# Optimization experiments

Measured on AMD Instinct MI355X. Metric: run time of the kernel, lower is better.

The kernel has to match this reference:

```python
import jax, jax.numpy as jnp
import numpy as np

ALPHA = 0.2  # leaky relu slope

def setup_inputs() -> dict:
    key = jax.random.key(0)
    k1, k2, k3, k4 = jax.random.split(key, 4)
    b, n, din, dout = 8, 2048, 256, 128
    x = jax.random.normal(k1, (b, n, din), dtype=jnp.float32)
    adj = jax.random.randint(k2, (b, n, n), 0, 2, dtype=jnp.int32)
    # xavier-ish scaling for params
    W = jax.random.normal(k3, (dout, din), dtype=jnp.float32) * (1.414 * (2.0 / (din + dout)) ** 0.5)
    a = jax.random.normal(k4, (2 * dout,), dtype=jnp.float32) * (1.414 * (2.0 / (2 * dout + 1)) ** 0.5)
    return {"x": x, "adj": adj, "W": W, "a": a}

def reference(x, adj, W, a):
    # x: [b, n, din]; W: [dout, din]; a: [2*dout]
    wh = jnp.einsum('bnd,od->bno', x, W)           # [b, n, dout]
    dout = W.shape[0]
    a_src, a_dst = a[:dout], a[dout:]
    # e_ij = leaky_relu(a_src . wh_i + a_dst . wh_j)  (decomposed, avoids O(n^2 * 2d) concat)
    e = (wh @ a_src)[:, :, None] + (wh @ a_dst)[:, None, :]  # [b, n, n]
    e = jnp.where(e >= 0, e, ALPHA * e)
    e = jnp.where(adj != 0, e, -jnp.inf)
    attention = jax.nn.softmax(e, axis=2)          # [b, n, n]
    out = jnp.einsum('bij,bjo->bio', attention, wh)  # [b, n, dout]
    return jax.nn.relu(out)
```

## Files before the change

kernel.cpp:

```cpp
#include <hip/hip_runtime.h>
#include <hip/hip_bf16.h>
#include <stdint.h>

#define GAT_ALPHA 0.2f
#define LOG2E 1.4426950408889634f

typedef __attribute__((ext_vector_type(8))) __bf16 bf16x8;
typedef __attribute__((ext_vector_type(4))) float f32x4;

union B8 {
  bf16x8 b;
  unsigned short u[8];
  unsigned int w[4];
  int4 i4;
};

__device__ __forceinline__ unsigned int pk2bf(float lo, float hi) {
  union { __hip_bfloat162 h; unsigned int u; } cv;
  cv.h = __float22bfloat162_rn(make_float2(lo, hi));
  return cv.u;
}

__global__ __launch_bounds__(256) void gat_pack(
    const int* __restrict__ adj, unsigned long long* __restrict__ mask) {
  const int tid = threadIdx.x;
  const int lane = tid & 63;
  const int wgl = (blockIdx.x * 256 + tid) >> 6;
  for (int it = wgl; it < 131072; it += 4096) {
    const size_t base = (size_t)it << 8;
    const int* p = adj + base + lane;
    int a0 = p[0], a1 = p[64], a2 = p[128], a3 = p[192];
    unsigned long long m0 = __ballot(a0 != 0);
    unsigned long long m1 = __ballot(a1 != 0);
    unsigned long long m2 = __ballot(a2 != 0);
    unsigned long long m3 = __ballot(a3 != 0);
    if (lane == 0) {
      unsigned long long* mp = mask + (base >> 6);
      mp[0] = m0; mp[1] = m1; mp[2] = m2; mp[3] = m3;
    }
  }
}

__global__ __launch_bounds__(256, 2) void gat_wh(
    const float* __restrict__ x, const float* __restrict__ W,
    const float* __restrict__ a, unsigned short* __restrict__ whTf,
    float* __restrict__ s_out, float* __restrict__ d_out) {
  __shared__ unsigned short WF[8][4][512];
  const int tid = threadIdx.x;
  const int wave = tid >> 6, lane = tid & 63;
  const int il = lane & 15, quad = lane >> 4;
  const int row0 = blockIdx.x * 64;
  const int i = row0 + wave * 16 + il;
  B8 av[8];
  {
    const float* xp = x + (size_t)i * 256 + quad * 8;
#pragma unroll
    for (int kc = 0; kc < 8; ++kc) {
      float4 lo = *(const float4*)(xp + kc * 32);
      float4 hi = *(const float4*)(xp + kc * 32 + 4);
      av[kc].w[0] = pk2bf(lo.x, lo.y);
      av[kc].w[1] = pk2bf(lo.z, lo.w);
      av[kc].w[2] = pk2bf(hi.x, hi.y);
      av[kc].w[3] = pk2bf(hi.z, hi.w);
    }
  }
  f32x4 acc[8];
#pragma unroll
  for (int nt = 0; nt < 8; ++nt) acc[nt] = (f32x4){0.f, 0.f, 0.f, 0.f};
#pragma unroll
  for (int h = 0; h < 2; ++h) {
    if (h) __syncthreads();
#pragma unroll
    for (int p = 0; p < 16; ++p) {
      const int f = p * 1024 + tid * 4;
      const int o = f >> 7, kk = f & 127;
      float4 v = *(const float4*)(W + o * 256 + h * 128 + kk);
      uint2 pk;
      pk.x = pk2bf(v.x, v.y);
      pk.y = pk2bf(v.z, v.w);
      *(uint2*)(&WF[o >> 4][kk >> 5][((o & 15) + (((kk & 31) >> 3) << 4)) * 8 + (kk & 7)]) = pk;
    }
    __syncthreads();
#pragma unroll
    for (int kl = 0; kl < 4; ++kl) {
      const int kc = h * 4 + kl;
#pragma unroll
      for (int nt = 0; nt < 8; ++nt) {
        B8 bv;
        bv.i4 = *(const int4*)(&WF[nt][kl][lane * 8]);
        acc[nt] = __builtin_amdgcn_mfma_f32_16x16x32_bf16(av[kc].b, bv.b, acc[nt], 0, 0, 0);
      }
    }
  }
  float asrc[8], adst[8];
#pragma unroll
  for (int nt = 0; nt < 8; ++nt) {
    asrc[nt] = a[nt * 16 + il];
    adst[nt] = a[128 + nt * 16 + il];
  }
  float sp[4], dp[4];
#pragma unroll
  for (int r = 0; r < 4; ++r) {
    float sv = 0.f, dv = 0.f;
#pragma unroll
    for (int nt = 0; nt < 8; ++nt) {
      sv += acc[nt][r] * asrc[nt];
      dv += acc[nt][r] * adst[nt];
    }
    sp[r] = sv; dp[r] = dv;
  }
#pragma unroll
  for (int off = 1; off <= 8; off <<= 1) {
#pragma unroll
    for (int r = 0; r < 4; ++r) {
      sp[r] += __shfl_xor(sp[r], off, 64);
      dp[r] += __shfl_xor(dp[r], off, 64);
    }
  }
  if (il == 0) {
#pragma unroll
    for (int r = 0; r < 4; ++r) {
      s_out[row0 + wave * 16 + quad * 4 + r] = sp[r];
      d_out[row0 + wave * 16 + quad * 4 + r] = dp[r];
    }
  }
  const int b = row0 >> 11;
  const int jc = ((row0 & 2047) >> 5) + (wave >> 1);
  const int kin = ((wave & 1) << 4) + (quad << 2);
  const int kq = kin >> 3, u0 = kin & 7;
#pragma unroll
  for (int nt = 0; nt < 8; ++nt) {
    uint2 pk;
    pk.x = pk2bf(acc[nt][0], acc[nt][1]);
    pk.y = pk2bf(acc[nt][2], acc[nt][3]);
    *(uint2*)(whTf + ((((size_t)(b * 64 + jc)) * 8 + nt) << 9) + ((il + (kq << 4)) << 3) + u0) = pk;
  }
}

__device__ __forceinline__ void dma16(const void* g, void* l) {
  __builtin_amdgcn_global_load_lds(
      (const __attribute__((address_space(1))) unsigned int*)g,
      (__attribute__((address_space(3))) unsigned int*)l, 16, 0, 0);
}

__global__ __launch_bounds__(256) void gat_attn(
    const unsigned int* __restrict__ mask32, const unsigned short* __restrict__ whTf,
    const float* __restrict__ s, const float* __restrict__ dvec,
    float* __restrict__ out) {
  __shared__ unsigned short vbuf[2][2][8][512];
  __shared__ unsigned int maskl[64][68];
  __shared__ float dl[2048];
  const int tid = threadIdx.x;
  const int wave = tid >> 6;
  const int lane = tid & 63;
  const int il = lane & 15;
  const int quad = lane >> 4;
  const int qo = quad << 3;
  const int b = blockIdx.x & 7;
  const int tile = blockIdx.x >> 3;
  const int rbase = tile * 64;
  {
    const float* dsrc = dvec + ((size_t)b << 11);
#pragma unroll
    for (int it = 0; it < 2; ++it) {
      const int idx = it * 1024 + tid * 4;
      float4 v = *(const float4*)(dsrc + idx);
      v.x *= LOG2E; v.y *= LOG2E; v.z *= LOG2E; v.w *= LOG2E;
      *(float4*)(&dl[idx]) = v;
    }
  }
  {
    const unsigned int* msrc = mask32 + (((size_t)b << 11) + rbase) * 64;
    const int c4 = (tid & 15) << 2;
#pragma unroll
    for (int kk = 0; kk < 4; ++kk) {
      const int r = (tid >> 4) + kk * 16;
      *(int4*)(&maskl[r][c4]) = *(const int4*)(msrc + r * 64 + c4);
    }
  }
  const unsigned short* whTb = whTf + (((size_t)b * 64) << 12);
  {
#pragma unroll
    for (int h = 0; h < 2; ++h) {
      const int nt = wave * 2 + h;
      dma16(whTb + ((size_t)(0 * 8 + nt) << 9) + (lane << 3), &vbuf[0][0][nt][0]);
      dma16(whTb + ((size_t)(1 * 8 + nt) << 9) + (lane << 3), &vbuf[0][1][nt][0]);
    }
  }
  const int i = rbase + wave * 16 + il;
  const size_t browi = ((size_t)b << 11) + i;
  const float svL = s[browi] * LOG2E;
  const int mrow = wave * 16 + il;

  f32x4 acc[8];
#pragma unroll
  for (int nt = 0; nt < 8; ++nt) acc[nt] = (f32x4){0.f, 0.f, 0.f, 0.f};
  float den = 0.f;
  __syncthreads();

#pragma unroll 2
  for (int T = 0; T < 32; ++T) {
    const int cur = T & 1, nxt = cur ^ 1;
    if (T < 31) {
#pragma unroll
      for (int h = 0; h < 2; ++h) {
        const int nt = wave * 2 + h;
        dma16(whTb + (((size_t)(2 * T + 2) * 8 + nt) << 9) + (lane << 3), &vbuf[nxt][0][nt][0]);
        dma16(whTb + (((size_t)(2 * T + 3) * 8 + nt) << 9) + (lane << 3), &vbuf[nxt][1][nt][0]);
      }
    }
#pragma unroll
    for (int c = 0; c < 2; ++c) {
      const int tt = 2 * T + c;
      const int j0 = tt * 32;
      const unsigned int mword = maskl[mrow][tt];
      const float4 d0 = *(const float4*)(&dl[j0 + qo]);
      const float4 d1 = *(const float4*)(&dl[j0 + qo + 4]);
      const float dd[8] = {d0.x, d0.y, d0.z, d0.w, d1.x, d1.y, d1.z, d1.w};
      B8 af[8];
#pragma unroll
      for (int nt = 0; nt < 8; ++nt)
        af[nt].i4 = *(const int4*)((const char*)&vbuf[cur][c][nt][0] + lane * 16);
      float pv[8];
#pragma unroll
      for (int u = 0; u < 8; ++u) {
        float t0 = svL + dd[u];
        float e2 = fmaxf(t0, GAT_ALPHA * t0);
        float p = __builtin_amdgcn_exp2f(e2);
        p = ((mword >> (qo + u)) & 1u) ? p : 0.f;
        den += p;
        pv[u] = p;
      }
      B8 pf;
      pf.w[0] = pk2bf(pv[0], pv[1]);
      pf.w[1] = pk2bf(pv[2], pv[3]);
      pf.w[2] = pk2bf(pv[4], pv[5]);
      pf.w[3] = pk2bf(pv[6], pv[7]);
#pragma unroll
      for (int nt = 0; nt < 8; ++nt)
        acc[nt] = __builtin_amdgcn_mfma_f32_16x16x32_bf16(af[nt].b, pf.b, acc[nt], 0, 0, 0);
    }
    __syncthreads();
  }
  den += __shfl_xor(den, 16, 64);
  den += __shfl_xor(den, 32, 64);
  const float inv = 1.0f / den;
  float* op = out + browi * 128;
#pragma unroll
  for (int nt = 0; nt < 8; ++nt) {
    float4 v;
    v.x = fmaxf(acc[nt][0] * inv, 0.f);
    v.y = fmaxf(acc[nt][1] * inv, 0.f);
    v.z = fmaxf(acc[nt][2] * inv, 0.f);
    v.w = fmaxf(acc[nt][3] * inv, 0.f);
    *(float4*)(op + nt * 16 + quad * 4) = v;
  }
}

extern "C" void kernel_launch(void* const* d_in, const int* in_sizes, int n_in,
                              void* d_out, int out_size, void* d_ws, size_t ws_size,
                              hipStream_t stream) {
  const float* x = (const float*)d_in[0];
  const int* adj = (const int*)d_in[1];
  const float* W = (const float*)d_in[2];
  const float* a = (const float*)d_in[3];
  float* out = (float*)d_out;
  unsigned short* whTf = (unsigned short*)d_ws;
  unsigned long long* mask = (unsigned long long*)((char*)d_ws + (size_t)4 * 1024 * 1024);
  float* s = (float*)((char*)d_ws + (size_t)8 * 1024 * 1024);
  float* dv = s + 16384;
  gat_pack<<<1024, 256, 0, stream>>>(adj, mask);
  gat_wh<<<256, 256, 0, stream>>>(x, W, a, whTf, s, dv);
  gat_attn<<<256, 256, 0, stream>>>((const unsigned int*)mask, whTf, s, dv, out);
}
```

Measured before the change: 255.5 us.

## Fuse adjacency bitmask packing into attention kernel, reading adj directly

Removes the separate gat_pack kernel and its mask buffer. The attention kernel now loads the int32 adjacency rows itself, one 64-column chunk per iteration, prefetching the next chunk into registers, and builds per-row bitmasks with wave ballots. This saves a kernel launch and the write and read of the packed mask. In exchange, the 128 MB adjacency read now sits inside the attention loop and adds 16 ballots per iteration, and the previous unroll-2 pragma is dropped.

```diff
diff --git a/kernel.cpp b/kernel.cpp
--- a/kernel.cpp
+++ b/kernel.cpp
@@ -21,24 +21,10 @@
   return cv.u;
 }
 
-__global__ __launch_bounds__(256) void gat_pack(
-    const int* __restrict__ adj, unsigned long long* __restrict__ mask) {
-  const int tid = threadIdx.x;
-  const int lane = tid & 63;
-  const int wgl = (blockIdx.x * 256 + tid) >> 6;
-  for (int it = wgl; it < 131072; it += 4096) {
-    const size_t base = (size_t)it << 8;
-    const int* p = adj + base + lane;
-    int a0 = p[0], a1 = p[64], a2 = p[128], a3 = p[192];
-    unsigned long long m0 = __ballot(a0 != 0);
-    unsigned long long m1 = __ballot(a1 != 0);
-    unsigned long long m2 = __ballot(a2 != 0);
-    unsigned long long m3 = __ballot(a3 != 0);
-    if (lane == 0) {
-      unsigned long long* mp = mask + (base >> 6);
-      mp[0] = m0; mp[1] = m1; mp[2] = m2; mp[3] = m3;
-    }
-  }
+__device__ __forceinline__ void dma16(const void* g, void* l) {
+  __builtin_amdgcn_global_load_lds(
+      (const __attribute__((address_space(1))) unsigned int*)g,
+      (__attribute__((address_space(3))) unsigned int*)l, 16, 0, 0);
 }
 
 __global__ __launch_bounds__(256, 2) void gat_wh(
@@ -137,18 +123,11 @@
   }
 }
 
-__device__ __forceinline__ void dma16(const void* g, void* l) {
-  __builtin_amdgcn_global_load_lds(
-      (const __attribute__((address_space(1))) unsigned int*)g,
-      (__attribute__((address_space(3))) unsigned int*)l, 16, 0, 0);
-}
-
 __global__ __launch_bounds__(256) void gat_attn(
-    const unsigned int* __restrict__ mask32, const unsigned short* __restrict__ whTf,
+    const int* __restrict__ adj, const unsigned short* __restrict__ whTf,
     const float* __restrict__ s, const float* __restrict__ dvec,
     float* __restrict__ out) {
   __shared__ unsigned short vbuf[2][2][8][512];
-  __shared__ unsigned int maskl[64][68];
   __shared__ float dl[2048];
   const int tid = threadIdx.x;
   const int wave = tid >> 6;
@@ -169,15 +148,10 @@
       *(float4*)(&dl[idx]) = v;
     }
   }
-  {
-    const unsigned int* msrc = mask32 + (((size_t)b << 11) + rbase) * 64;
-    const int c4 = (tid & 15) << 2;
-#pragma unroll
-    for (int kk = 0; kk < 4; ++kk) {
-      const int r = (tid >> 4) + kk * 16;
-      *(int4*)(&maskl[r][c4]) = *(const int4*)(msrc + r * 64 + c4);
-    }
-  }
+  const int* aro = adj + ((((size_t)b << 11) + rbase + wave * 16) << 11);
+  int lv[16];
+#pragma unroll
+  for (int r = 0; r < 16; ++r) lv[r] = aro[(r << 11) + lane];
   const unsigned short* whTb = whTf + (((size_t)b * 64) << 12);
   {
 #pragma unroll
@@ -190,18 +164,27 @@
   const int i = rbase + wave * 16 + il;
   const size_t browi = ((size_t)b << 11) + i;
   const float svL = s[browi] * LOG2E;
-  const int mrow = wave * 16 + il;
-
+  unsigned long long mcur;
+  {
+    unsigned long long sel = __ballot(lv[0] != 0);
+#pragma unroll
+    for (int r = 1; r < 16; ++r) {
+      const unsigned long long mm = __ballot(lv[r] != 0);
+      sel = (il == r) ? mm : sel;
+    }
+    mcur = sel;
+  }
   f32x4 acc[8];
 #pragma unroll
   for (int nt = 0; nt < 8; ++nt) acc[nt] = (f32x4){0.f, 0.f, 0.f, 0.f};
   float den = 0.f;
   __syncthreads();
 
-#pragma unroll 2
   for (int T = 0; T < 32; ++T) {
     const int cur = T & 1, nxt = cur ^ 1;
     if (T < 31) {
+#pragma unroll
+      for (int r = 0; r < 16; ++r) lv[r] = aro[(r << 11) + (T + 1) * 64 + lane];
 #pragma unroll
       for (int h = 0; h < 2; ++h) {
         const int nt = wave * 2 + h;
@@ -211,9 +194,8 @@
     }
 #pragma unroll
     for (int c = 0; c < 2; ++c) {
-      const int tt = 2 * T + c;
-      const int j0 = tt * 32;
-      const unsigned int mword = maskl[mrow][tt];
+      const int j0 = (2 * T + c) * 32;
+      const unsigned int mq = (unsigned int)(mcur >> (32 * c + qo));
       const float4 d0 = *(const float4*)(&dl[j0 + qo]);
       const float4 d1 = *(const float4*)(&dl[j0 + qo + 4]);
       const float dd[8] = {d0.x, d0.y, d0.z, d0.w, d1.x, d1.y, d1.z, d1.w};
@@ -227,7 +209,7 @@
         float t0 = svL + dd[u];
         float e2 = fmaxf(t0, GAT_ALPHA * t0);
         float p = __builtin_amdgcn_exp2f(e2);
-        p = ((mword >> (qo + u)) & 1u) ? p : 0.f;
+        p = ((mq >> u) & 1u) ? p : 0.f;
         den += p;
         pv[u] = p;
       }
@@ -239,6 +221,15 @@
 #pragma unroll
       for (int nt = 0; nt < 8; ++nt)
         acc[nt] = __builtin_amdgcn_mfma_f32_16x16x32_bf16(af[nt].b, pf.b, acc[nt], 0, 0, 0);
+    }
+    if (T < 31) {
+      unsigned long long sel = __ballot(lv[0] != 0);
+#pragma unroll
+      for (int r = 1; r < 16; ++r) {
+        const unsigned long long mm = __ballot(lv[r] != 0);
+        sel = (il == r) ? mm : sel;
+      }
+      mcur = sel;
     }
     __syncthreads();
   }
@@ -266,10 +257,8 @@
   const float* a = (const float*)d_in[3];
   float* out = (float*)d_out;
   unsigned short* whTf = (unsigned short*)d_ws;
-  unsigned long long* mask = (unsigned long long*)((char*)d_ws + (size_t)4 * 1024 * 1024);
-  float* s = (float*)((char*)d_ws + (size_t)8 * 1024 * 1024);
+  float* s = (float*)((char*)d_ws + (size_t)4 * 1024 * 1024);
   float* dv = s + 16384;
-  gat_pack<<<1024, 256, 0, stream>>>(adj, mask);
   gat_wh<<<256, 256, 0, stream>>>(x, W, a, whTf, s, dv);
-  gat_attn<<<256, 256, 0, stream>>>((const unsigned int*)mask, whTf, s, dv, out);
-}
+  gat_attn<<<256, 256, 0, stream>>>(adj, whTf, s, dv, out);
+}
```

Result: faster. 236.3 us (-7.5%).
